# Kernel optimization log

Hardware: AMD Instinct MI355X
Metric: run time of the kernel (lower is better)

## Reference

```python
import jax, jax.numpy as jnp
import numpy as np

B, K2, C, H, W = 8, 9, 1, 256, 1216


def setup_inputs() -> dict:
    key = jax.random.key(0)
    k1, k2 = jax.random.split(key)
    affinity = jax.random.normal(k1, (B, K2, H, W), dtype=jnp.float32)
    feature = jax.random.normal(k2, (B, C, H, W), dtype=jnp.float32)
    return {"affinity": affinity, "feature": feature, "times": 24}


def reference(affinity, feature, times):
    # affinity: [B, 9, H, W]; feature: [B, C, H, W]
    b, k2, h, w = affinity.shape
    a_abs = jnp.abs(affinity)
    a_norm = a_abs / a_abs.sum(axis=1, keepdims=True)  # per-pixel normalized weights [B,9,H,W]

    def step(feat, _):
        fp = jnp.pad(feat, ((0, 0), (0, 0), (1, 1), (1, 1)))  # 3x3 stencil, pad=1
        # Stack the 9 shifted views: [B, 9, C, H, W] (row-major over 3x3 window,
        # matching index = pad_h*3 + pad_w in the torch loop)
        shifts = jnp.stack(
            [fp[:, :, i:i + h, j:j + w] for i in range(3) for j in range(3)],
            axis=1,
        )
        out = jnp.einsum('bncij,bnij->bcij', shifts, a_norm)
        return out, None

    feat, _ = jax.lax.scan(step, feature, None, length=times)
    return feat
```

## Files before the change

### kernel.cpp

```cpp
#include <hip/hip_runtime.h>

#define BB 8
#define HH 256
#define WW 1216
#define TIMES 24

#define KF 4
#define TSZ 26
#define FSZ 34
#define NT 512
#define NFPIX (FSZ*FSZ)
#define TGX 47
#define TGY 10
#define NTILES (TGX*TGY)

#define WPIX 1024
#define WELEM (9*WPIX)
#define WBYTES (WELEM*2)
#define WCHUNKS (WBYTES/256)

static const size_t HW = (size_t)HH * WW;
#define DEQ (1.0f/65535.0f)

#define LDS_BARRIER() do { asm volatile("s_waitcnt lgkmcnt(0)" ::: "memory"); \
                           __builtin_amdgcn_s_barrier(); } while (0)

__device__ __forceinline__ void gload_lds4(const unsigned int* g, void* l) {
    __builtin_amdgcn_global_load_lds(
        (const __attribute__((address_space(1))) void*)g,
        (__attribute__((address_space(3))) void*)l, 4, 0, 0);
}

#define STEPW(BC, W0, W1, o0, o1) do {                                     \
    const float* _c0 = (BC) + tb0;                                         \
    const float* _c1 = (BC) + tb1;                                         \
    (o0) = W0[0]*_c0[0]       + W0[1]*_c0[1]         + W0[2]*_c0[2]        \
         + W0[3]*_c0[FSZ]     + W0[4]*_c0[FSZ+1]     + W0[5]*_c0[FSZ+2]    \
         + W0[6]*_c0[2*FSZ]   + W0[7]*_c0[2*FSZ+1]   + W0[8]*_c0[2*FSZ+2]; \
    (o1) = W1[0]*_c1[0]       + W1[1]*_c1[1]         + W1[2]*_c1[2]        \
         + W1[3]*_c1[FSZ]     + W1[4]*_c1[FSZ+1]     + W1[5]*_c1[FSZ+2]    \
         + W1[6]*_c1[2*FSZ]   + W1[7]*_c1[2*FSZ+1]   + W1[8]*_c1[2*FSZ+2]; \
} while (0)

__global__ __launch_bounds__(256) void prep_kernel(const float* __restrict__ aff,
                                                   unsigned short* __restrict__ wq) {
    const int tile = blockIdx.x;
    const int b    = blockIdx.y;
    const int ty   = tile / TGX, tx = tile - ty * TGX;
    const int x0   = tx * TSZ,   y0 = ty * TSZ;
    const float* ap = aff + (size_t)b * 9 * HW;
    unsigned short* op = wq + (size_t)(tile * BB + b) * WELEM;

#pragma unroll
    for (int s = 0; s < 4; ++s) {
        int p  = threadIdx.x + s * 256;
        int wy = p >> 5, wx = p & 31;
        int gy = y0 - (KF - 1) + wy;
        int gx = x0 - (KF - 1) + wx;
        bool in = (unsigned)gy < (unsigned)HH && (unsigned)gx < (unsigned)WW;
        int qi[9];
        if (in) {
            const float* pp = ap + (size_t)gy * WW + gx;
            float v[9], ssum = 0.0f;
#pragma unroll
            for (int n = 0; n < 9; ++n) { v[n] = fabsf(pp[(size_t)n * HW]); ssum += v[n]; }
            float sc = 65535.0f / ssum;
            int tot = 0, m = 0; float vmax = v[0];
#pragma unroll
            for (int n = 0; n < 9; ++n) {
                qi[n] = (int)(v[n] * sc + 0.5f);
                tot += qi[n];
                if (v[n] > vmax) { vmax = v[n]; m = n; }
            }
            int delta = 65535 - tot;
#pragma unroll
            for (int n = 0; n < 9; ++n) qi[n] += (n == m) ? delta : 0;
        } else {
#pragma unroll
            for (int n = 0; n < 9; ++n) qi[n] = 0;
        }
#pragma unroll
        for (int n = 0; n < 9; ++n) op[n * WPIX + p] = (unsigned short)qi[n];
    }
}

__global__ __launch_bounds__(NT, 4) void fused4_kernel(const unsigned short* __restrict__ wq,
                                                       const float* __restrict__ src,
                                                       float* __restrict__ dst) {
    __shared__ float S[NFPIX], P[NFPIX], Q[NFPIX];
    __shared__ unsigned short Wl[WELEM];

    const int t    = threadIdx.x;
    const int wv   = t >> 6;
    const int lane = t & 63;
    const int tile = blockIdx.x;
    const int ty   = tile / TGX, tx = tile - ty * TGX;
    const int x0   = tx * TSZ,   y0 = ty * TSZ;

    const int wx  = t & 31;
    const int wy0 = t >> 5;
    const int wy1 = wy0 + 16;
    const int gx  = x0 - (KF - 1) + wx;
    const int gy0 = y0 - (KF - 1) + wy0;
    const int gy1 = gy0 + 16;
    const bool in0 = (unsigned)gy0 < (unsigned)HH && (unsigned)gx < (unsigned)WW;
    const bool in1 = (unsigned)gy1 < (unsigned)HH && (unsigned)gx < (unsigned)WW;
    const int  tb0 = wy0 * FSZ + wx;
    const int  tb1 = tb0 + 16 * FSZ;
    const int  cw0 = (wy0 + 1) * FSZ + (wx + 1);
    const int  cw1 = cw0 + 16 * FSZ;

    int foff[3]; bool fok[3];
#pragma unroll
    for (int r = 0; r < 3; ++r) {
        int p  = t + r * NT;
        int fy = p / FSZ, fx = p - fy * FSZ;
        int gfy = y0 - KF + fy, gfx = x0 - KF + fx;
        fok[r]  = (p < NFPIX) && (unsigned)gfy < (unsigned)HH && (unsigned)gfx < (unsigned)WW;
        foff[r] = gfy * WW + gfx;
    }

#pragma unroll
    for (int r = 0; r < 3; ++r) {
        int p = t + r * NT;
        if (p < NFPIX) { P[p] = 0.0f; Q[p] = 0.0f; }
    }

    {
        const unsigned int* w32 = (const unsigned int*)(wq + (size_t)(tile * BB) * WELEM);
        for (int c = wv; c < WCHUNKS; c += 8)
            gload_lds4(w32 + c * 64 + lane, (char*)Wl + c * 256);
    }
#pragma unroll
    for (int r = 0; r < 3; ++r) {
        int p = t + r * NT;
        if (p < NFPIX) S[p] = fok[r] ? src[foff[r]] : 0.0f;
    }
    __syncthreads();

    for (int b = 0; b < BB; ++b) {
        float w0[9], w1[9];
#pragma unroll
        for (int n = 0; n < 9; ++n) {
            w0[n] = (float)Wl[n * WPIX + t]       * DEQ;
            w1[n] = (float)Wl[n * WPIX + t + 512] * DEQ;
        }
        LDS_BARRIER();

        const bool pf = (b + 1 < BB);
        float fn[3];
        if (pf) {
            const unsigned int* w32 =
                (const unsigned int*)(wq + (size_t)(tile * BB + b + 1) * WELEM);
            for (int c = wv; c < WCHUNKS; c += 8)
                gload_lds4(w32 + c * 64 + lane, (char*)Wl + c * 256);
            const float* sp = src + (size_t)(b + 1) * HW;
#pragma unroll
            for (int r = 0; r < 3; ++r) fn[r] = fok[r] ? sp[foff[r]] : 0.0f;
        }
        __builtin_amdgcn_sched_barrier(0);

        float r0, r1;
        STEPW(S, w0, w1, r0, r1);
        P[cw0] = r0; P[cw1] = r1;
        LDS_BARRIER();
        STEPW(P, w0, w1, r0, r1);
        Q[cw0] = r0; Q[cw1] = r1;
        LDS_BARRIER();
        if (pf) {
#pragma unroll
            for (int r = 0; r < 3; ++r) {
                int p = t + r * NT;
                if (p < NFPIX) S[p] = fn[r];
            }
        }
        STEPW(Q, w0, w1, r0, r1);
        P[cw0] = r0; P[cw1] = r1;
        LDS_BARRIER();
        STEPW(P, w0, w1, r0, r1);

        asm volatile("s_waitcnt vmcnt(0)" ::: "memory");
        LDS_BARRIER();

        const size_t base = (size_t)b * HW;
        if ((unsigned)(wx - (KF - 1)) < (unsigned)TSZ) {
            if ((unsigned)(wy0 - (KF - 1)) < (unsigned)TSZ && in0)
                dst[base + (size_t)gy0 * WW + gx] = r0;
            if ((unsigned)(wy1 - (KF - 1)) < (unsigned)TSZ && in1)
                dst[base + (size_t)gy1 * WW + gx] = r1;
        }
    }
}

extern "C" void kernel_launch(void* const* d_in, const int* in_sizes, int n_in,
                              void* d_out, int out_size, void* d_ws, size_t ws_size,
                              hipStream_t stream) {
    const float* affinity = (const float*)d_in[0];
    const float* feature  = (const float*)d_in[1];

    unsigned short* wq = (unsigned short*)d_ws;
    float* bufA = (float*)((char*)d_ws + (size_t)NTILES * BB * WBYTES);
    float* bufO = (float*)d_out;

    prep_kernel<<<dim3(NTILES, BB), dim3(256), 0, stream>>>(affinity, wq);

    const int NL = TIMES / KF;
    const float* src = feature;
    for (int l = 0; l < NL; ++l) {
        float* dst = (l & 1) ? bufO : bufA;
        fused4_kernel<<<dim3(NTILES), dim3(NT), 0, stream>>>(wq, src, dst);
        src = dst;
    }
}
```

Measured before the change: 195.0 us.

## Give each thread two vertically adjacent pixels sharing stencil rows via paired LDS reads

Each thread now computes two vertically adjacent output pixels instead of two pixels 16 rows apart, so the two 3x3 windows share two rows. This cuts LDS reads from 18 to 12, issued as six ds_read2_b32 plus one ds_write2_b32 in inline asm. The prep kernel interleaves the quantized weights so a thread's two pixels sit in one 32-bit word, halving weight LDS reads. The risk is that the explicit waitcnt and sched barriers in the asm stop the compiler from interleaving loads with math, and the new access pattern may cause more LDS bank conflicts.

```diff
diff --git a/kernel.cpp b/kernel.cpp
--- a/kernel.cpp
+++ b/kernel.cpp
@@ -22,8 +22,14 @@
 static const size_t HW = (size_t)HH * WW;
 #define DEQ (1.0f/65535.0f)
 
+typedef float f32x2 __attribute__((ext_vector_type(2)));
+
 #define LDS_BARRIER() do { asm volatile("s_waitcnt lgkmcnt(0)" ::: "memory"); \
                            __builtin_amdgcn_s_barrier(); } while (0)
+
+__device__ __forceinline__ unsigned lds_off(const void* p) {
+    return (unsigned)(size_t)(const __attribute__((address_space(3))) void*)p;
+}
 
 __device__ __forceinline__ void gload_lds4(const unsigned int* g, void* l) {
     __builtin_amdgcn_global_load_lds(
@@ -31,15 +37,30 @@
         (__attribute__((address_space(3))) void*)l, 4, 0, 0);
 }
 
-#define STEPW(BC, W0, W1, o0, o1) do {                                     \
-    const float* _c0 = (BC) + tb0;                                         \
-    const float* _c1 = (BC) + tb1;                                         \
-    (o0) = W0[0]*_c0[0]       + W0[1]*_c0[1]         + W0[2]*_c0[2]        \
-         + W0[3]*_c0[FSZ]     + W0[4]*_c0[FSZ+1]     + W0[5]*_c0[FSZ+2]    \
-         + W0[6]*_c0[2*FSZ]   + W0[7]*_c0[2*FSZ+1]   + W0[8]*_c0[2*FSZ+2]; \
-    (o1) = W1[0]*_c1[0]       + W1[1]*_c1[1]         + W1[2]*_c1[2]        \
-         + W1[3]*_c1[FSZ]     + W1[4]*_c1[FSZ+1]     + W1[5]*_c1[FSZ+2]    \
-         + W1[6]*_c1[2*FSZ]   + W1[7]*_c1[2*FSZ+1]   + W1[8]*_c1[2*FSZ+2]; \
+#define STEPV(BC, o0, o1) do {                                                        \
+    unsigned _ab = lds_off((BC) + tb0);                                               \
+    f32x2 _v0,_v1,_v2,_v3,_v4,_v5;                                                    \
+    asm volatile("ds_read2_b32 %0, %1 offset0:0   offset1:1"  : "=v"(_v0) : "v"(_ab));\
+    asm volatile("ds_read2_b32 %0, %1 offset0:2   offset1:34" : "=v"(_v1) : "v"(_ab));\
+    asm volatile("ds_read2_b32 %0, %1 offset0:35  offset1:36" : "=v"(_v2) : "v"(_ab));\
+    asm volatile("ds_read2_b32 %0, %1 offset0:68  offset1:69" : "=v"(_v3) : "v"(_ab));\
+    asm volatile("ds_read2_b32 %0, %1 offset0:70  offset1:102": "=v"(_v4) : "v"(_ab));\
+    asm volatile("ds_read2_b32 %0, %1 offset0:103 offset1:104": "=v"(_v5) : "v"(_ab));\
+    asm volatile("s_waitcnt lgkmcnt(0)" ::: "memory");                                \
+    __builtin_amdgcn_sched_barrier(0);                                                \
+    float _t00=_v0.x,_t01=_v0.y,_t02=_v1.x;                                           \
+    float _t10=_v1.y,_t11=_v2.x,_t12=_v2.y;                                           \
+    float _t20=_v3.x,_t21=_v3.y,_t22=_v4.x;                                           \
+    float _t30=_v4.y,_t31=_v5.x,_t32=_v5.y;                                           \
+    (o0) = w0[0]*_t00+w0[1]*_t01+w0[2]*_t02 + w0[3]*_t10+w0[4]*_t11+w0[5]*_t12        \
+         + w0[6]*_t20+w0[7]*_t21+w0[8]*_t22;                                          \
+    (o1) = w1[0]*_t10+w1[1]*_t11+w1[2]*_t12 + w1[3]*_t20+w1[4]*_t21+w1[5]*_t22        \
+         + w1[6]*_t30+w1[7]*_t31+w1[8]*_t32;                                          \
+} while (0)
+
+#define STORE2(BN) do {                                                               \
+    asm volatile("ds_write2_b32 %0, %1, %2 offset0:0 offset1:34"                      \
+        :: "v"(lds_off((BN) + cw0)), "v"(r0), "v"(r1) : "memory");                    \
 } while (0)
 
 __global__ __launch_bounds__(256) void prep_kernel(const float* __restrict__ aff,
@@ -79,16 +100,17 @@
 #pragma unroll
             for (int n = 0; n < 9; ++n) qi[n] = 0;
         }
-#pragma unroll
-        for (int n = 0; n < 9; ++n) op[n * WPIX + p] = (unsigned short)qi[n];
-    }
-}
-
-__global__ __launch_bounds__(NT, 4) void fused4_kernel(const unsigned short* __restrict__ wq,
+        int pi = ((p >> 6) << 6) + ((p & 31) << 1) + ((p >> 5) & 1);
+#pragma unroll
+        for (int n = 0; n < 9; ++n) op[n * WPIX + pi] = (unsigned short)qi[n];
+    }
+}
+
+__global__ __launch_bounds__(NT, 4) void fused4_kernel(const unsigned int* __restrict__ wq,
                                                        const float* __restrict__ src,
                                                        float* __restrict__ dst) {
     __shared__ float S[NFPIX], P[NFPIX], Q[NFPIX];
-    __shared__ unsigned short Wl[WELEM];
+    __shared__ unsigned int Wl[WELEM / 2];
 
     const int t    = threadIdx.x;
     const int wv   = t >> 6;
@@ -98,17 +120,15 @@
     const int x0   = tx * TSZ,   y0 = ty * TSZ;
 
     const int wx  = t & 31;
-    const int wy0 = t >> 5;
-    const int wy1 = wy0 + 16;
+    const int wy0 = (t >> 5) * 2;
     const int gx  = x0 - (KF - 1) + wx;
     const int gy0 = y0 - (KF - 1) + wy0;
-    const int gy1 = gy0 + 16;
+    const int gy1 = gy0 + 1;
     const bool in0 = (unsigned)gy0 < (unsigned)HH && (unsigned)gx < (unsigned)WW;
     const bool in1 = (unsigned)gy1 < (unsigned)HH && (unsigned)gx < (unsigned)WW;
     const int  tb0 = wy0 * FSZ + wx;
-    const int  tb1 = tb0 + 16 * FSZ;
     const int  cw0 = (wy0 + 1) * FSZ + (wx + 1);
-    const int  cw1 = cw0 + 16 * FSZ;
+    const int  widx = (t >> 5) * 32 + (t & 31);
 
     int foff[3]; bool fok[3];
 #pragma unroll
@@ -127,7 +147,7 @@
     }
 
     {
-        const unsigned int* w32 = (const unsigned int*)(wq + (size_t)(tile * BB) * WELEM);
+        const unsigned int* w32 = wq + (size_t)(tile * BB) * (WELEM / 2);
         for (int c = wv; c < WCHUNKS; c += 8)
             gload_lds4(w32 + c * 64 + lane, (char*)Wl + c * 256);
     }
@@ -142,16 +162,16 @@
         float w0[9], w1[9];
 #pragma unroll
         for (int n = 0; n < 9; ++n) {
-            w0[n] = (float)Wl[n * WPIX + t]       * DEQ;
-            w1[n] = (float)Wl[n * WPIX + t + 512] * DEQ;
+            unsigned u = Wl[n * (WPIX / 2) + widx];
+            w0[n] = (float)(u & 0xffffu) * DEQ;
+            w1[n] = (float)(u >> 16)     * DEQ;
         }
         LDS_BARRIER();
 
         const bool pf = (b + 1 < BB);
         float fn[3];
         if (pf) {
-            const unsigned int* w32 =
-                (const unsigned int*)(wq + (size_t)(tile * BB + b + 1) * WELEM);
+            const unsigned int* w32 = wq + (size_t)(tile * BB + b + 1) * (WELEM / 2);
             for (int c = wv; c < WCHUNKS; c += 8)
                 gload_lds4(w32 + c * 64 + lane, (char*)Wl + c * 256);
             const float* sp = src + (size_t)(b + 1) * HW;
@@ -161,11 +181,11 @@
         __builtin_amdgcn_sched_barrier(0);
 
         float r0, r1;
-        STEPW(S, w0, w1, r0, r1);
-        P[cw0] = r0; P[cw1] = r1;
-        LDS_BARRIER();
-        STEPW(P, w0, w1, r0, r1);
-        Q[cw0] = r0; Q[cw1] = r1;
+        STEPV(S, r0, r1);
+        STORE2(P);
+        LDS_BARRIER();
+        STEPV(P, r0, r1);
+        STORE2(Q);
         LDS_BARRIER();
         if (pf) {
 #pragma unroll
@@ -174,19 +194,19 @@
                 if (p < NFPIX) S[p] = fn[r];
             }
         }
-        STEPW(Q, w0, w1, r0, r1);
-        P[cw0] = r0; P[cw1] = r1;
-        LDS_BARRIER();
-        STEPW(P, w0, w1, r0, r1);
+        STEPV(Q, r0, r1);
+        STORE2(P);
+        LDS_BARRIER();
+        STEPV(P, r0, r1);
 
         asm volatile("s_waitcnt vmcnt(0)" ::: "memory");
         LDS_BARRIER();
 
         const size_t base = (size_t)b * HW;
         if ((unsigned)(wx - (KF - 1)) < (unsigned)TSZ) {
-            if ((unsigned)(wy0 - (KF - 1)) < (unsigned)TSZ && in0)
+            if ((unsigned)(wy0     - (KF - 1)) < (unsigned)TSZ && in0)
                 dst[base + (size_t)gy0 * WW + gx] = r0;
-            if ((unsigned)(wy1 - (KF - 1)) < (unsigned)TSZ && in1)
+            if ((unsigned)(wy0 + 1 - (KF - 1)) < (unsigned)TSZ && in1)
                 dst[base + (size_t)gy1 * WW + gx] = r1;
         }
     }
@@ -208,7 +228,7 @@
     const float* src = feature;
     for (int l = 0; l < NL; ++l) {
         float* dst = (l & 1) ? bufO : bufA;
-        fused4_kernel<<<dim3(NTILES), dim3(NT), 0, stream>>>(wq, src, dst);
+        fused4_kernel<<<dim3(NTILES), dim3(NT), 0, stream>>>((const unsigned int*)wq, src, dst);
         src = dst;
     }
 }
```

Measured after the change: 181.0 us. 1.08x faster.
